# Performance work log

Hardware: AMD Instinct MI355X
Metric: run time of the kernel (lower is better)

Reference implementation:

```python
import jax, jax.numpy as jnp
import numpy as np

MAX_M = 16
B, H, N_LEN = 16, 256, 4096


def _ref_dft_np(n, h):
    a = np.arange(n)
    M = np.exp(-2j * np.pi * np.outer(a, a) / n)  # (n, n) complex
    M = np.broadcast_to(M, (h, n, n))
    return np.ascontiguousarray(np.stack([M.real, M.imag], axis=-1)).astype(np.float32)


def setup_inputs() -> dict:
    key = jax.random.key(0)
    k1, k2 = jax.random.split(key)
    x_real = jax.random.normal(k1, (B, H, N_LEN), dtype=jnp.float32)
    x_imag = jax.random.normal(k2, (B, H, N_LEN), dtype=jnp.float32)
    # Learned DFT matrices are initialized to the exact reference DFT matrices
    # (learn_additive=False path in the torch module).
    return {
        "x_real": x_real,
        "x_imag": x_imag,
        "mat_2": jnp.asarray(_ref_dft_np(2, H)),
        "mat_4": jnp.asarray(_ref_dft_np(4, H)),
        "mat_8": jnp.asarray(_ref_dft_np(8, H)),
        "mat_16": jnp.asarray(_ref_dft_np(16, H)),
        "N": N_LEN,
    }


def _twiddle(n, m):
    na = jnp.arange(n)[:, None]
    ma = jnp.arange(m)[None, :]
    return jnp.exp((-2j * jnp.pi / (n * m)) * (na * ma).astype(jnp.float32))  # (n, m)


def _cooley_tukey(k, n, m, mats):
    # k: (..., n*m) complex; FFT of length n*m along last dim.
    k = k.reshape(k.shape[:-1] + (m, n))  # '... (m n) -> ... m n'
    # n m-length DFTs along rows: mats[m] is (H, m, m), broadcasts over leading dims.
    k_f = jnp.einsum('...mo,...on->...mn', mats[m], k)
    twi = _twiddle(n, m).astype(k_f.dtype)  # (n, m)
    k_f = jnp.einsum('nm,...mn->...nm', twi, k_f)  # transpose + twiddle
    if n <= MAX_M:
        k_f = jnp.einsum('...no,...om->...nm', mats[n], k_f)
    else:
        k_f = jnp.moveaxis(k_f, -1, -3)  # '... h n m -> ... m h n'
        k_f = _cooley_tukey(k_f, n // MAX_M, MAX_M, mats)
        k_f = jnp.moveaxis(k_f, -3, -1)  # '... m h n -> ... h n m'
    return k_f.reshape(k_f.shape[:-2] + (k_f.shape[-2] * k_f.shape[-1],))


def reference(x_real, x_imag, mat_2, mat_4, mat_8, mat_16, N):
    x = x_real + 1j * x_imag  # (B, H, N) complex64
    mats = {p: (mm[..., 0] + 1j * mm[..., 1])
            for p, mm in ((2, mat_2), (4, mat_4), (8, mat_8), (16, mat_16))}
    out = _cooley_tukey(x, N // MAX_M, MAX_M, mats)  # (B, H, N) complex
    # view_as_real representation of the complex FFT output
    return jnp.stack([out.real, out.imag], axis=-1)  # (B, H, N, 2)
```

## Files before the change

kernel.cpp:

```cpp
#include <hip/hip_runtime.h>
#include <stdint.h>

typedef _Float16 f16x8 __attribute__((ext_vector_type(8)));
typedef float    f32x4 __attribute__((ext_vector_type(4)));

union FragU { unsigned u[4]; f16x8 h; };

__device__ __forceinline__ unsigned pkh(float a, float b) {
    return __builtin_bit_cast(unsigned, __builtin_amdgcn_cvt_pkrtz(a, b));
}
__device__ __forceinline__ unsigned short h16(float a) {
    return __builtin_bit_cast(unsigned short, (_Float16)a);
}

#define MFMA(A, B, C) __builtin_amdgcn_mfma_f32_16x16x32_f16((A).h, (B).h, (C), 0, 0, 0)

#define K1 (-1.5339807878856412e-03f)
#define K2 (-2.4543692606170259e-02f)

__global__ __launch_bounds__(256, 4) void fft4096_mfma(
    const float* __restrict__ xre, const float* __restrict__ xim,
    const float* __restrict__ mat16, float* __restrict__ out, int H)
{
    __shared__ __align__(16) unsigned char smem[32768];

    const int t = threadIdx.x;
    const int w = t >> 6;
    const int l = t & 63;
    const int g = l >> 4;
    const int c = l & 15;
    const int bh = blockIdx.x;
    const int h  = bh % H;
    const size_t base = (size_t)bh * 4096;

    float xr[4][4], xi[4][4];
#pragma unroll
    for (int p = 0; p < 4; ++p) {
        const int col = (4 * w + p) * 16 + c;
#pragma unroll
        for (int jj = 0; jj < 4; ++jj) {
            xr[p][jj] = xre[base + (size_t)((4 * g + jj) * 256 + col)];
            xi[p][jj] = xim[base + (size_t)((4 * g + jj) * 256 + col)];
        }
    }

    const float* Mb = mat16 + (size_t)h * 512 + (size_t)c * 32 + g * 8;
    const float4 mf0 = *(const float4*)Mb;
    const float4 mf1 = *(const float4*)(Mb + 4);
    const unsigned mrA = pkh(mf0.x, mf0.z), mrB = pkh(mf1.x, mf1.z);
    const unsigned miA = pkh(mf0.y, mf0.w), miB = pkh(mf1.y, mf1.w);
    const unsigned nmiA = miA ^ 0x80008000u, nmiB = miB ^ 0x80008000u;

    FragU Afrag;
    Afrag.u[0] = mrA; Afrag.u[1] = mrB; Afrag.u[2] = miA; Afrag.u[3] = miB;
    FragU BMr;
    BMr.u[0] = mrA; BMr.u[1] = mrB; BMr.u[2] = nmiA; BMr.u[3] = nmiB;
    FragU BMi;
    BMi.u[0] = miA; BMi.u[1] = miB; BMi.u[2] = mrA; BMi.u[3] = mrB;

    const f32x4 zero = {0.f, 0.f, 0.f, 0.f};

    f32x4 s1r[4], s1i[4];
#pragma unroll
    for (int p = 0; p < 4; ++p) {
        const unsigned rp0 = pkh(xr[p][0], xr[p][1]), rp1 = pkh(xr[p][2], xr[p][3]);
        const unsigned ip0 = pkh(xi[p][0], xi[p][1]), ip1 = pkh(xi[p][2], xi[p][3]);
        const unsigned np0 = ip0 ^ 0x80008000u, np1 = ip1 ^ 0x80008000u;
        FragU Br; Br.u[0] = rp0; Br.u[1] = rp1; Br.u[2] = np0; Br.u[3] = np1;
        FragU Bi; Bi.u[0] = ip0; Bi.u[1] = ip1; Bi.u[2] = rp0; Bi.u[3] = rp1;
        s1r[p] = MFMA(Afrag, Br, zero);
        s1i[p] = MFMA(Afrag, Bi, zero);
    }
#pragma unroll
    for (int p = 0; p < 4; ++p) {
        const int j = (4 * w + p) * 16 + c;
        float sb, cb, ss, cs;
        __sincosf(K1 * (float)(j * 4 * g), &sb, &cb);
        __sincosf(K1 * (float)j, &ss, &cs);
#pragma unroll
        for (int reg = 0; reg < 4; ++reg) {
            const float yr = s1r[p][reg], yi = s1i[p][reg];
            s1r[p][reg] = yr * cb - yi * sb;
            s1i[p][reg] = yr * sb + yi * cb;
            const float nc = cb * cs - sb * ss;
            const float ns = cb * ss + sb * cs;
            cb = nc; sb = ns;
        }
    }
#pragma unroll
    for (int reg = 0; reg < 4; ++reg) {
        const int m1 = 4 * g + reg;
        const int half = m1 * 256 + c * 16 + 4 * ((w ^ (c >> 2) ^ reg) & 3);
        uint2 vr, vi;
        vr.x = pkh(s1r[0][reg], s1r[1][reg]); vr.y = pkh(s1r[2][reg], s1r[3][reg]);
        vi.x = pkh(s1i[0][reg], s1i[1][reg]); vi.y = pkh(s1i[2][reg], s1i[3][reg]);
        *(uint2*)(smem + half * 2)        = vr;
        *(uint2*)(smem + 8192 + half * 2) = vi;
    }
    __syncthreads();

    f32x4 s2r[4], s2i[4];
#pragma unroll
    for (int p = 0; p < 4; ++p) {
        const int m1 = 4 * w + p;
        const int half = m1 * 256 + c * 16 + 4 * ((g ^ (c >> 2) ^ p) & 3);
        const uint2 rp = *(const uint2*)(smem + half * 2);
        const uint2 ip = *(const uint2*)(smem + 8192 + half * 2);
        FragU Br; Br.u[0] = rp.x; Br.u[1] = rp.y;
        Br.u[2] = ip.x ^ 0x80008000u; Br.u[3] = ip.y ^ 0x80008000u;
        FragU Bi; Bi.u[0] = ip.x; Bi.u[1] = ip.y; Bi.u[2] = rp.x; Bi.u[3] = rp.y;
        s2r[p] = MFMA(Afrag, Br, zero);
        s2i[p] = MFMA(Afrag, Bi, zero);
    }
    float twc[4], tws[4];
    {
        float sb, cb, ss, cs;
        __sincosf(K2 * (float)(c * 4 * g), &sb, &cb);
        __sincosf(K2 * (float)c, &ss, &cs);
#pragma unroll
        for (int reg = 0; reg < 4; ++reg) {
            twc[reg] = cb; tws[reg] = sb;
            const float nc = cb * cs - sb * ss;
            const float ns = cb * ss + sb * cs;
            cb = nc; sb = ns;
        }
    }
#pragma unroll
    for (int p = 0; p < 4; ++p) {
#pragma unroll
        for (int reg = 0; reg < 4; ++reg) {
            const float yr = s2r[p][reg], yi = s2i[p][reg];
            s2r[p][reg] = yr * twc[reg] - yi * tws[reg];
            s2i[p][reg] = yr * tws[reg] + yi * twc[reg];
        }
    }
#pragma unroll
    for (int reg = 0; reg < 4; ++reg) {
        const int m2 = 4 * g + reg;
#pragma unroll
        for (int p = 0; p < 4; ++p) {
            const int spos = (((4 * w + p) * 16 + c) ^ (g << 4)) ^ (reg << 2);
            const int half = m2 * 256 + spos;
            *(unsigned short*)(smem + 16384 + half * 2) = h16(s2r[p][reg]);
            *(unsigned short*)(smem + 24576 + half * 2) = h16(s2i[p][reg]);
        }
    }
    __syncthreads();

    FragU Aup[4];
#pragma unroll
    for (int p = 0; p < 4; ++p) {
        const int spos = ((((4 * w + p) * 16 + 4 * g) ^ (((c >> 2) & 3) << 4))
                          ^ ((c & 3) << 2));
        const int half = c * 256 + spos;
        const uint2 hr = *(const uint2*)(smem + 16384 + half * 2);
        const uint2 hi = *(const uint2*)(smem + 24576 + half * 2);
        Aup[p].u[0] = hr.x; Aup[p].u[1] = hr.y;
        Aup[p].u[2] = hi.x; Aup[p].u[3] = hi.y;
    }
    __syncthreads();

    f32x4 vR[4], vI[4];
#pragma unroll
    for (int p = 0; p < 4; ++p) {
        vR[p] = MFMA(Aup[p], BMr, zero);
        vI[p] = MFMA(Aup[p], BMi, zero);
    }

    {
        const int swz = (c & 7) << 1;
#pragma unroll
        for (int reg = 0; reg < 4; ++reg) {
            const int i0 = (((4 * g + reg) * 16 + 4 * w) ^ swz);
            const int i1 = (((4 * g + reg) * 16 + 4 * w + 2) ^ swz);
            const f32x4 a = {vR[0][reg], vI[0][reg], vR[1][reg], vI[1][reg]};
            const f32x4 b = {vR[2][reg], vI[2][reg], vR[3][reg], vI[3][reg]};
            *(f32x4*)(smem + (size_t)(c * 256 + i0) * 8) = a;
            *(f32x4*)(smem + (size_t)(c * 256 + i1) * 8) = b;
        }
    }
    __syncthreads();

    f32x4* __restrict__ og4 = (f32x4*)out;
#pragma unroll
    for (int it = 0; it < 8; ++it) {
        const int jr = 2 * it + (t >> 7);
        const int u  = (t & 127) * 2;
        const int is = u ^ ((jr & 7) << 1);
        const f32x4 v = *(const f32x4*)(smem + (size_t)(jr * 256 + is) * 8);
        __builtin_nontemporal_store(v, &og4[(base + (size_t)(jr * 256 + u)) >> 1]);
    }
}

extern "C" void kernel_launch(void* const* d_in, const int* in_sizes, int n_in,
                              void* d_out, int out_size, void* d_ws, size_t ws_size,
                              hipStream_t stream)
{
    const float* xre = (const float*)d_in[0];
    const float* xim = (const float*)d_in[1];
    const float* m16 = (const float*)d_in[5];
    const int H  = in_sizes[5] / 512;
    const int BH = in_sizes[0] / 4096;
    fft4096_mfma<<<dim3(BH), dim3(256), 0, stream>>>(
        xre, xim, m16, (float*)d_out, H);
}
```

Measured before the change: 47.06 us.

## Process two rows per block and prefetch the second row during the first

Each block now handles two (batch, head) rows, rowA and rowA+BH/2, which share the same head because BH/2 is a multiple of H, so the DFT matrix fragments and twiddles are loaded once. The second row's global loads are issued after the first sync of row A, so they overlap with row A's remaining compute and stores. The grid is halved, which means fewer blocks and less parallelism on the device, and the extra prefetch registers raise register pressure. The code assumes BH is even and that BH/2 is divisible by H.

```diff
diff --git a/kernel.cpp b/kernel.cpp
--- a/kernel.cpp
+++ b/kernel.cpp
@@ -20,7 +20,7 @@
 
 __global__ __launch_bounds__(256, 4) void fft4096_mfma(
     const float* __restrict__ xre, const float* __restrict__ xim,
-    const float* __restrict__ mat16, float* __restrict__ out, int H)
+    const float* __restrict__ mat16, float* __restrict__ out, int H, int BH)
 {
     __shared__ __align__(16) unsigned char smem[32768];
 
@@ -29,18 +29,21 @@
     const int l = t & 63;
     const int g = l >> 4;
     const int c = l & 15;
-    const int bh = blockIdx.x;
-    const int h  = bh % H;
-    const size_t base = (size_t)bh * 4096;
-
-    float xr[4][4], xi[4][4];
+
+    const int rowA = blockIdx.x;
+    const int rowB = rowA + (BH >> 1);
+    const int h    = rowA % H;
+    const size_t baseA = (size_t)rowA * 4096;
+    const size_t baseB = (size_t)rowB * 4096;
+
+    float xAr[4][4], xAi[4][4], xBr[4][4], xBi[4][4];
 #pragma unroll
     for (int p = 0; p < 4; ++p) {
         const int col = (4 * w + p) * 16 + c;
 #pragma unroll
         for (int jj = 0; jj < 4; ++jj) {
-            xr[p][jj] = xre[base + (size_t)((4 * g + jj) * 256 + col)];
-            xi[p][jj] = xim[base + (size_t)((4 * g + jj) * 256 + col)];
+            xAr[p][jj] = xre[baseA + (size_t)((4 * g + jj) * 256 + col)];
+            xAi[p][jj] = xim[baseA + (size_t)((4 * g + jj) * 256 + col)];
         }
     }
 
@@ -58,60 +61,6 @@
     FragU BMi;
     BMi.u[0] = miA; BMi.u[1] = miB; BMi.u[2] = mrA; BMi.u[3] = mrB;
 
-    const f32x4 zero = {0.f, 0.f, 0.f, 0.f};
-
-    f32x4 s1r[4], s1i[4];
-#pragma unroll
-    for (int p = 0; p < 4; ++p) {
-        const unsigned rp0 = pkh(xr[p][0], xr[p][1]), rp1 = pkh(xr[p][2], xr[p][3]);
-        const unsigned ip0 = pkh(xi[p][0], xi[p][1]), ip1 = pkh(xi[p][2], xi[p][3]);
-        const unsigned np0 = ip0 ^ 0x80008000u, np1 = ip1 ^ 0x80008000u;
-        FragU Br; Br.u[0] = rp0; Br.u[1] = rp1; Br.u[2] = np0; Br.u[3] = np1;
-        FragU Bi; Bi.u[0] = ip0; Bi.u[1] = ip1; Bi.u[2] = rp0; Bi.u[3] = rp1;
-        s1r[p] = MFMA(Afrag, Br, zero);
-        s1i[p] = MFMA(Afrag, Bi, zero);
-    }
-#pragma unroll
-    for (int p = 0; p < 4; ++p) {
-        const int j = (4 * w + p) * 16 + c;
-        float sb, cb, ss, cs;
-        __sincosf(K1 * (float)(j * 4 * g), &sb, &cb);
-        __sincosf(K1 * (float)j, &ss, &cs);
-#pragma unroll
-        for (int reg = 0; reg < 4; ++reg) {
-            const float yr = s1r[p][reg], yi = s1i[p][reg];
-            s1r[p][reg] = yr * cb - yi * sb;
-            s1i[p][reg] = yr * sb + yi * cb;
-            const float nc = cb * cs - sb * ss;
-            const float ns = cb * ss + sb * cs;
-            cb = nc; sb = ns;
-        }
-    }
-#pragma unroll
-    for (int reg = 0; reg < 4; ++reg) {
-        const int m1 = 4 * g + reg;
-        const int half = m1 * 256 + c * 16 + 4 * ((w ^ (c >> 2) ^ reg) & 3);
-        uint2 vr, vi;
-        vr.x = pkh(s1r[0][reg], s1r[1][reg]); vr.y = pkh(s1r[2][reg], s1r[3][reg]);
-        vi.x = pkh(s1i[0][reg], s1i[1][reg]); vi.y = pkh(s1i[2][reg], s1i[3][reg]);
-        *(uint2*)(smem + half * 2)        = vr;
-        *(uint2*)(smem + 8192 + half * 2) = vi;
-    }
-    __syncthreads();
-
-    f32x4 s2r[4], s2i[4];
-#pragma unroll
-    for (int p = 0; p < 4; ++p) {
-        const int m1 = 4 * w + p;
-        const int half = m1 * 256 + c * 16 + 4 * ((g ^ (c >> 2) ^ p) & 3);
-        const uint2 rp = *(const uint2*)(smem + half * 2);
-        const uint2 ip = *(const uint2*)(smem + 8192 + half * 2);
-        FragU Br; Br.u[0] = rp.x; Br.u[1] = rp.y;
-        Br.u[2] = ip.x ^ 0x80008000u; Br.u[3] = ip.y ^ 0x80008000u;
-        FragU Bi; Bi.u[0] = ip.x; Bi.u[1] = ip.y; Bi.u[2] = rp.x; Bi.u[3] = rp.y;
-        s2r[p] = MFMA(Afrag, Br, zero);
-        s2i[p] = MFMA(Afrag, Bi, zero);
-    }
     float twc[4], tws[4];
     {
         float sb, cb, ss, cs;
@@ -125,70 +74,150 @@
             cb = nc; sb = ns;
         }
     }
-#pragma unroll
-    for (int p = 0; p < 4; ++p) {
+
+    const f32x4 zero = {0.f, 0.f, 0.f, 0.f};
+    f32x4* __restrict__ og4 = (f32x4*)out;
+
+#pragma unroll
+    for (int r = 0; r < 2; ++r) {
+        const size_t base = r ? baseB : baseA;
+
+        f32x4 s1r[4], s1i[4];
+#pragma unroll
+        for (int p = 0; p < 4; ++p) {
+            float r0, r1, r2, r3, i0, i1, i2, i3;
+            if (r == 0) {
+                r0 = xAr[p][0]; r1 = xAr[p][1]; r2 = xAr[p][2]; r3 = xAr[p][3];
+                i0 = xAi[p][0]; i1 = xAi[p][1]; i2 = xAi[p][2]; i3 = xAi[p][3];
+            } else {
+                r0 = xBr[p][0]; r1 = xBr[p][1]; r2 = xBr[p][2]; r3 = xBr[p][3];
+                i0 = xBi[p][0]; i1 = xBi[p][1]; i2 = xBi[p][2]; i3 = xBi[p][3];
+            }
+            const unsigned rp0 = pkh(r0, r1), rp1 = pkh(r2, r3);
+            const unsigned ip0 = pkh(i0, i1), ip1 = pkh(i2, i3);
+            const unsigned np0 = ip0 ^ 0x80008000u, np1 = ip1 ^ 0x80008000u;
+            FragU Br; Br.u[0] = rp0; Br.u[1] = rp1; Br.u[2] = np0; Br.u[3] = np1;
+            FragU Bi; Bi.u[0] = ip0; Bi.u[1] = ip1; Bi.u[2] = rp0; Bi.u[3] = rp1;
+            s1r[p] = MFMA(Afrag, Br, zero);
+            s1i[p] = MFMA(Afrag, Bi, zero);
+        }
+#pragma unroll
+        for (int p = 0; p < 4; ++p) {
+            const int j = (4 * w + p) * 16 + c;
+            float sb, cb, ss, cs;
+            __sincosf(K1 * (float)(j * 4 * g), &sb, &cb);
+            __sincosf(K1 * (float)j, &ss, &cs);
+#pragma unroll
+            for (int reg = 0; reg < 4; ++reg) {
+                const float yr = s1r[p][reg], yi = s1i[p][reg];
+                s1r[p][reg] = yr * cb - yi * sb;
+                s1i[p][reg] = yr * sb + yi * cb;
+                const float nc = cb * cs - sb * ss;
+                const float ns = cb * ss + sb * cs;
+                cb = nc; sb = ns;
+            }
+        }
 #pragma unroll
         for (int reg = 0; reg < 4; ++reg) {
-            const float yr = s2r[p][reg], yi = s2i[p][reg];
-            s2r[p][reg] = yr * twc[reg] - yi * tws[reg];
-            s2i[p][reg] = yr * tws[reg] + yi * twc[reg];
-        }
-    }
-#pragma unroll
-    for (int reg = 0; reg < 4; ++reg) {
-        const int m2 = 4 * g + reg;
-#pragma unroll
-        for (int p = 0; p < 4; ++p) {
-            const int spos = (((4 * w + p) * 16 + c) ^ (g << 4)) ^ (reg << 2);
-            const int half = m2 * 256 + spos;
-            *(unsigned short*)(smem + 16384 + half * 2) = h16(s2r[p][reg]);
-            *(unsigned short*)(smem + 24576 + half * 2) = h16(s2i[p][reg]);
-        }
-    }
-    __syncthreads();
-
-    FragU Aup[4];
-#pragma unroll
-    for (int p = 0; p < 4; ++p) {
-        const int spos = ((((4 * w + p) * 16 + 4 * g) ^ (((c >> 2) & 3) << 4))
-                          ^ ((c & 3) << 2));
-        const int half = c * 256 + spos;
-        const uint2 hr = *(const uint2*)(smem + 16384 + half * 2);
-        const uint2 hi = *(const uint2*)(smem + 24576 + half * 2);
-        Aup[p].u[0] = hr.x; Aup[p].u[1] = hr.y;
-        Aup[p].u[2] = hi.x; Aup[p].u[3] = hi.y;
-    }
-    __syncthreads();
-
-    f32x4 vR[4], vI[4];
-#pragma unroll
-    for (int p = 0; p < 4; ++p) {
-        vR[p] = MFMA(Aup[p], BMr, zero);
-        vI[p] = MFMA(Aup[p], BMi, zero);
-    }
-
-    {
-        const int swz = (c & 7) << 1;
+            const int m1 = 4 * g + reg;
+            const int half = m1 * 256 + c * 16 + 4 * ((w ^ (c >> 2) ^ reg) & 3);
+            uint2 vr, vi;
+            vr.x = pkh(s1r[0][reg], s1r[1][reg]); vr.y = pkh(s1r[2][reg], s1r[3][reg]);
+            vi.x = pkh(s1i[0][reg], s1i[1][reg]); vi.y = pkh(s1i[2][reg], s1i[3][reg]);
+            *(uint2*)(smem + half * 2)        = vr;
+            *(uint2*)(smem + 8192 + half * 2) = vi;
+        }
+        __syncthreads();
+
+        if (r == 0) {
+#pragma unroll
+            for (int p = 0; p < 4; ++p) {
+                const int col = (4 * w + p) * 16 + c;
+#pragma unroll
+                for (int jj = 0; jj < 4; ++jj) {
+                    xBr[p][jj] = xre[baseB + (size_t)((4 * g + jj) * 256 + col)];
+                    xBi[p][jj] = xim[baseB + (size_t)((4 * g + jj) * 256 + col)];
+                }
+            }
+        }
+
+        f32x4 s2r[4], s2i[4];
+#pragma unroll
+        for (int p = 0; p < 4; ++p) {
+            const int m1 = 4 * w + p;
+            const int half = m1 * 256 + c * 16 + 4 * ((g ^ (c >> 2) ^ p) & 3);
+            const uint2 rp = *(const uint2*)(smem + half * 2);
+            const uint2 ip = *(const uint2*)(smem + 8192 + half * 2);
+            FragU Br; Br.u[0] = rp.x; Br.u[1] = rp.y;
+            Br.u[2] = ip.x ^ 0x80008000u; Br.u[3] = ip.y ^ 0x80008000u;
+            FragU Bi; Bi.u[0] = ip.x; Bi.u[1] = ip.y; Bi.u[2] = rp.x; Bi.u[3] = rp.y;
+            s2r[p] = MFMA(Afrag, Br, zero);
+            s2i[p] = MFMA(Afrag, Bi, zero);
+        }
+#pragma unroll
+        for (int p = 0; p < 4; ++p) {
+#pragma unroll
+            for (int reg = 0; reg < 4; ++reg) {
+                const float yr = s2r[p][reg], yi = s2i[p][reg];
+                s2r[p][reg] = yr * twc[reg] - yi * tws[reg];
+                s2i[p][reg] = yr * tws[reg] + yi * twc[reg];
+            }
+        }
 #pragma unroll
         for (int reg = 0; reg < 4; ++reg) {
-            const int i0 = (((4 * g + reg) * 16 + 4 * w) ^ swz);
-            const int i1 = (((4 * g + reg) * 16 + 4 * w + 2) ^ swz);
-            const f32x4 a = {vR[0][reg], vI[0][reg], vR[1][reg], vI[1][reg]};
-            const f32x4 b = {vR[2][reg], vI[2][reg], vR[3][reg], vI[3][reg]};
-            *(f32x4*)(smem + (size_t)(c * 256 + i0) * 8) = a;
-            *(f32x4*)(smem + (size_t)(c * 256 + i1) * 8) = b;
-        }
-    }
-    __syncthreads();
-
-    f32x4* __restrict__ og4 = (f32x4*)out;
-#pragma unroll
-    for (int it = 0; it < 8; ++it) {
-        const int jr = 2 * it + (t >> 7);
-        const int u  = (t & 127) * 2;
-        const int is = u ^ ((jr & 7) << 1);
-        const f32x4 v = *(const f32x4*)(smem + (size_t)(jr * 256 + is) * 8);
-        __builtin_nontemporal_store(v, &og4[(base + (size_t)(jr * 256 + u)) >> 1]);
+            const int m2 = 4 * g + reg;
+#pragma unroll
+            for (int p = 0; p < 4; ++p) {
+                const int spos = (((4 * w + p) * 16 + c) ^ (g << 4)) ^ (reg << 2);
+                const int half = m2 * 256 + spos;
+                *(unsigned short*)(smem + 16384 + half * 2) = h16(s2r[p][reg]);
+                *(unsigned short*)(smem + 24576 + half * 2) = h16(s2i[p][reg]);
+            }
+        }
+
+        FragU Aup[4];
+#pragma unroll
+        for (int p = 0; p < 4; ++p) {
+            const int spos = ((((4 * w + p) * 16 + 4 * g) ^ (((c >> 2) & 3) << 4))
+                              ^ ((c & 3) << 2));
+            const int half = c * 256 + spos;
+            const uint2 hr = *(const uint2*)(smem + 16384 + half * 2);
+            const uint2 hi = *(const uint2*)(smem + 24576 + half * 2);
+            Aup[p].u[0] = hr.x; Aup[p].u[1] = hr.y;
+            Aup[p].u[2] = hi.x; Aup[p].u[3] = hi.y;
+        }
+        __syncthreads();
+
+        f32x4 vR[4], vI[4];
+#pragma unroll
+        for (int p = 0; p < 4; ++p) {
+            vR[p] = MFMA(Aup[p], BMr, zero);
+            vI[p] = MFMA(Aup[p], BMi, zero);
+        }
+
+        {
+            const int swz = (c & 7) << 1;
+#pragma unroll
+            for (int reg = 0; reg < 4; ++reg) {
+                const int i0 = (((4 * g + reg) * 16 + 4 * w) ^ swz);
+                const int i1 = (((4 * g + reg) * 16 + 4 * w + 2) ^ swz);
+                const f32x4 a = {vR[0][reg], vI[0][reg], vR[1][reg], vI[1][reg]};
+                const f32x4 b = {vR[2][reg], vI[2][reg], vR[3][reg], vI[3][reg]};
+                *(f32x4*)(smem + (size_t)(c * 256 + i0) * 8) = a;
+                *(f32x4*)(smem + (size_t)(c * 256 + i1) * 8) = b;
+            }
+        }
+        __syncthreads();
+
+#pragma unroll
+        for (int it = 0; it < 8; ++it) {
+            const int jr = 2 * it + (t >> 7);
+            const int u  = (t & 127) * 2;
+            const int is = u ^ ((jr & 7) << 1);
+            const f32x4 v = *(const f32x4*)(smem + (size_t)(jr * 256 + is) * 8);
+            __builtin_nontemporal_store(v, &og4[(base + (size_t)(jr * 256 + u)) >> 1]);
+        }
+        if (r == 0) __syncthreads();
     }
 }
 
@@ -201,6 +230,6 @@
     const float* m16 = (const float*)d_in[5];
     const int H  = in_sizes[5] / 512;
     const int BH = in_sizes[0] / 4096;
-    fft4096_mfma<<<dim3(BH), dim3(256), 0, stream>>>(
-        xre, xim, m16, (float*)d_out, H);
-}
+    fft4096_mfma<<<dim3(BH / 2), dim3(256), 0, stream>>>(
+        xre, xim, m16, (float*)d_out, H, BH);
+}
```

New measurement: 64.22 us. +36.5%, slower.

## Halve shared memory by aliasing buffers and staging output in fp16

Applied to the files above, without the earlier changes.

Shared memory drops from 32 KB to 16 KB. The second-stage buffers now reuse the first-stage region, with an extra barrier after the stage-2 loads, and the final output transpose is staged as packed fp16 complex pairs instead of fp32. Launch bounds are raised to 6 blocks per CU to use the extra occupancy. The fp16 staging of outputs adds rounding error to the final results, and the extra barrier adds synchronisation cost.

```diff
diff --git a/kernel.cpp b/kernel.cpp
--- a/kernel.cpp
+++ b/kernel.cpp
@@ -5,6 +5,7 @@
 typedef float    f32x4 __attribute__((ext_vector_type(4)));
 
 union FragU { unsigned u[4]; f16x8 h; };
+union H2U  { unsigned u; _Float16 h[2]; };
 
 __device__ __forceinline__ unsigned pkh(float a, float b) {
     return __builtin_bit_cast(unsigned, __builtin_amdgcn_cvt_pkrtz(a, b));
@@ -18,11 +19,11 @@
 #define K1 (-1.5339807878856412e-03f)
 #define K2 (-2.4543692606170259e-02f)
 
-__global__ __launch_bounds__(256, 4) void fft4096_mfma(
+__global__ __launch_bounds__(256, 6) void fft4096_mfma(
     const float* __restrict__ xre, const float* __restrict__ xim,
     const float* __restrict__ mat16, float* __restrict__ out, int H)
 {
-    __shared__ __align__(16) unsigned char smem[32768];
+    __shared__ __align__(16) unsigned char smem[16384];
 
     const int t = threadIdx.x;
     const int w = t >> 6;
@@ -99,21 +100,25 @@
     }
     __syncthreads();
 
-    f32x4 s2r[4], s2i[4];
+    uint2 rp[4], ip[4];
 #pragma unroll
     for (int p = 0; p < 4; ++p) {
         const int m1 = 4 * w + p;
         const int half = m1 * 256 + c * 16 + 4 * ((g ^ (c >> 2) ^ p) & 3);
-        const uint2 rp = *(const uint2*)(smem + half * 2);
-        const uint2 ip = *(const uint2*)(smem + 8192 + half * 2);
-        FragU Br; Br.u[0] = rp.x; Br.u[1] = rp.y;
-        Br.u[2] = ip.x ^ 0x80008000u; Br.u[3] = ip.y ^ 0x80008000u;
-        FragU Bi; Bi.u[0] = ip.x; Bi.u[1] = ip.y; Bi.u[2] = rp.x; Bi.u[3] = rp.y;
+        rp[p] = *(const uint2*)(smem + half * 2);
+        ip[p] = *(const uint2*)(smem + 8192 + half * 2);
+    }
+    f32x4 s2r[4], s2i[4];
+#pragma unroll
+    for (int p = 0; p < 4; ++p) {
+        FragU Br; Br.u[0] = rp[p].x; Br.u[1] = rp[p].y;
+        Br.u[2] = ip[p].x ^ 0x80008000u; Br.u[3] = ip[p].y ^ 0x80008000u;
+        FragU Bi; Bi.u[0] = ip[p].x; Bi.u[1] = ip[p].y; Bi.u[2] = rp[p].x; Bi.u[3] = rp[p].y;
         s2r[p] = MFMA(Afrag, Br, zero);
         s2i[p] = MFMA(Afrag, Bi, zero);
     }
-    float twc[4], tws[4];
     {
+        float twc[4], tws[4];
         float sb, cb, ss, cs;
         __sincosf(K2 * (float)(c * 4 * g), &sb, &cb);
         __sincosf(K2 * (float)c, &ss, &cs);
@@ -124,16 +129,18 @@
             const float ns = cb * ss + sb * cs;
             cb = nc; sb = ns;
         }
-    }
-#pragma unroll
-    for (int p = 0; p < 4; ++p) {
-#pragma unroll
-        for (int reg = 0; reg < 4; ++reg) {
-            const float yr = s2r[p][reg], yi = s2i[p][reg];
-            s2r[p][reg] = yr * twc[reg] - yi * tws[reg];
-            s2i[p][reg] = yr * tws[reg] + yi * twc[reg];
-        }
-    }
+#pragma unroll
+        for (int p = 0; p < 4; ++p) {
+#pragma unroll
+            for (int reg = 0; reg < 4; ++reg) {
+                const float yr = s2r[p][reg], yi = s2i[p][reg];
+                s2r[p][reg] = yr * twc[reg] - yi * tws[reg];
+                s2i[p][reg] = yr * tws[reg] + yi * twc[reg];
+            }
+        }
+    }
+    __syncthreads();
+
 #pragma unroll
     for (int reg = 0; reg < 4; ++reg) {
         const int m2 = 4 * g + reg;
@@ -141,8 +148,8 @@
         for (int p = 0; p < 4; ++p) {
             const int spos = (((4 * w + p) * 16 + c) ^ (g << 4)) ^ (reg << 2);
             const int half = m2 * 256 + spos;
-            *(unsigned short*)(smem + 16384 + half * 2) = h16(s2r[p][reg]);
-            *(unsigned short*)(smem + 24576 + half * 2) = h16(s2i[p][reg]);
+            *(unsigned short*)(smem + half * 2)        = h16(s2r[p][reg]);
+            *(unsigned short*)(smem + 8192 + half * 2) = h16(s2i[p][reg]);
         }
     }
     __syncthreads();
@@ -153,8 +160,8 @@
         const int spos = ((((4 * w + p) * 16 + 4 * g) ^ (((c >> 2) & 3) << 4))
                           ^ ((c & 3) << 2));
         const int half = c * 256 + spos;
-        const uint2 hr = *(const uint2*)(smem + 16384 + half * 2);
-        const uint2 hi = *(const uint2*)(smem + 24576 + half * 2);
+        const uint2 hr = *(const uint2*)(smem + half * 2);
+        const uint2 hi = *(const uint2*)(smem + 8192 + half * 2);
         Aup[p].u[0] = hr.x; Aup[p].u[1] = hr.y;
         Aup[p].u[2] = hi.x; Aup[p].u[3] = hi.y;
     }
@@ -168,27 +175,30 @@
     }
 
     {
-        const int swz = (c & 7) << 1;
+        const int key = (c & 7) ^ ((g & 1) << 3);
 #pragma unroll
         for (int reg = 0; reg < 4; ++reg) {
-            const int i0 = (((4 * g + reg) * 16 + 4 * w) ^ swz);
-            const int i1 = (((4 * g + reg) * 16 + 4 * w + 2) ^ swz);
-            const f32x4 a = {vR[0][reg], vI[0][reg], vR[1][reg], vI[1][reg]};
-            const f32x4 b = {vR[2][reg], vI[2][reg], vR[3][reg], vI[3][reg]};
-            *(f32x4*)(smem + (size_t)(c * 256 + i0) * 8) = a;
-            *(f32x4*)(smem + (size_t)(c * 256 + i1) * 8) = b;
+            const int Pl = (4 * g + reg) * 8 + 2 * w;
+            const int P0 = Pl ^ key, P1 = (Pl + 1) ^ key;
+            uint2 v0, v1;
+            v0.x = pkh(vR[0][reg], vI[0][reg]); v0.y = pkh(vR[1][reg], vI[1][reg]);
+            v1.x = pkh(vR[2][reg], vI[2][reg]); v1.y = pkh(vR[3][reg], vI[3][reg]);
+            *(uint2*)(smem + (size_t)(c * 256 + 2 * P0) * 4) = v0;
+            *(uint2*)(smem + (size_t)(c * 256 + 2 * P1) * 4) = v1;
         }
     }
     __syncthreads();
 
     f32x4* __restrict__ og4 = (f32x4*)out;
+    const int tl = t & 127;
 #pragma unroll
     for (int it = 0; it < 8; ++it) {
         const int jr = 2 * it + (t >> 7);
-        const int u  = (t & 127) * 2;
-        const int is = u ^ ((jr & 7) << 1);
-        const f32x4 v = *(const f32x4*)(smem + (size_t)(jr * 256 + is) * 8);
-        __builtin_nontemporal_store(v, &og4[(base + (size_t)(jr * 256 + u)) >> 1]);
+        const int Ps = tl ^ (jr & 7) ^ (((tl >> 5) & 1) << 3);
+        const uint2 pv = *(const uint2*)(smem + (size_t)(jr * 256 + 2 * Ps) * 4);
+        H2U a, b; a.u = pv.x; b.u = pv.y;
+        const f32x4 v = {(float)a.h[0], (float)a.h[1], (float)b.h[0], (float)b.h[1]};
+        __builtin_nontemporal_store(v, &og4[(base >> 1) + (size_t)(jr * 128 + tl)]);
     }
 }
 
```

Measured after the change: 45.92 us. 1.02x faster.
